# Optimization experiments

Hardware: AMD Instinct MI355X
Metric: run time of the kernel (lower is better)

## Reference

```python
import jax, jax.numpy as jnp
import numpy as np

DIM = 1024
N_HEAD = 16
HEAD_DIM = DIM // N_HEAD
HIDDEN = 4 * DIM
EPS = 1e-6
NEG = -1e9


def setup_inputs() -> dict:
    key = jax.random.key(0)
    ks = jax.random.split(key, 9)
    B, T = 2, 2048
    x = jax.random.normal(ks[0], (B, T, DIM), dtype=jnp.float32)
    # additive causal mask [T, T]
    mask = jnp.where(jnp.tril(jnp.ones((T, T), dtype=bool)), 0.0, NEG).astype(jnp.float32)
    s = 0.02
    wq = jax.random.normal(ks[1], (DIM, DIM), dtype=jnp.float32) * s
    wk = jax.random.normal(ks[2], (DIM, DIM), dtype=jnp.float32) * s
    wv = jax.random.normal(ks[3], (DIM, DIM), dtype=jnp.float32) * s
    wo = jax.random.normal(ks[4], (DIM, DIM), dtype=jnp.float32) * s
    w1 = jax.random.normal(ks[5], (DIM, HIDDEN), dtype=jnp.float32) * s
    w2 = jax.random.normal(ks[6], (HIDDEN, DIM), dtype=jnp.float32) * s
    g_attn = jnp.ones((DIM,), dtype=jnp.float32)
    g_ffn = jnp.ones((DIM,), dtype=jnp.float32)
    return {"x": x, "mask": mask, "wq": wq, "wk": wk, "wv": wv, "wo": wo,
            "w1": w1, "w2": w2, "g_attn": g_attn, "g_ffn": g_ffn}


def _rmsnorm(x, g):
    norm = jax.lax.rsqrt(jnp.mean(jnp.square(x), axis=-1, keepdims=True) + EPS)
    return (x * norm) * g


def _attention(x, mask, wq, wk, wv, wo):
    B, T, C = x.shape
    # project and split heads: [B, H, T, D]
    q = (x @ wq).reshape(B, T, N_HEAD, HEAD_DIM).transpose(0, 2, 1, 3)
    k = (x @ wk).reshape(B, T, N_HEAD, HEAD_DIM).transpose(0, 2, 1, 3)
    v = (x @ wv).reshape(B, T, N_HEAD, HEAD_DIM).transpose(0, 2, 1, 3)
    attn = jnp.einsum('bhtd,bhsd->bhts', q, k) / np.sqrt(HEAD_DIM).astype(np.float32)
    attn = attn + mask  # broadcast [T,T] over [B,H,T,T]
    p = jax.nn.softmax(attn, axis=-1)
    out = jnp.einsum('bhts,bhsd->bhtd', p, v)
    out = out.transpose(0, 2, 1, 3).reshape(B, T, C)
    return out @ wo


def reference(x, mask, wq, wk, wv, wo, w1, w2, g_attn, g_ffn):
    x = x + _attention(_rmsnorm(x, g_attn), mask, wq, wk, wv, wo)
    h = _rmsnorm(x, g_ffn)
    return x + (jax.nn.silu(h @ w1) @ w2)
```

## Files before the change

kernel.cpp:

```cpp
#include <hip/hip_runtime.h>
#include <hip/hip_bf16.h>
#include <cstdint>
#include <cstddef>

#define DIM    1024
#define NHEAD  16
#define HDIM   64
#define HIDDEN 4096
#define TSEQ   2048
#define TOKENS 4096

typedef __attribute__((ext_vector_type(4))) float  f32x4;
typedef __attribute__((ext_vector_type(8))) short  short8;
typedef __attribute__((ext_vector_type(8))) __bf16 bf16x8;

__device__ __forceinline__ short f2bf(float f) {
    union { float f; uint32_t u; } v; v.f = f;
    uint32_t u = v.u;
    uint32_t r = (u + 0x7fffu + ((u >> 16) & 1u)) >> 16;
    return (short)r;
}

__device__ __forceinline__ float bf2f(short s) {
    uint32_t u = ((uint32_t)(uint16_t)s) << 16;
    return __builtin_bit_cast(float, u);
}

__device__ __forceinline__ f32x4 mfma_bf16(short8 a, short8 b, f32x4 c) {
    return __builtin_amdgcn_mfma_f32_16x16x32_bf16(
        __builtin_bit_cast(bf16x8, a), __builtin_bit_cast(bf16x8, b), c, 0, 0, 0);
}

__device__ __forceinline__ void barrier_lds() {
    asm volatile("s_waitcnt lgkmcnt(0)\n\ts_barrier" ::: "memory");
}

__global__ __launch_bounds__(256) void transpose_w(
    const float* __restrict__ W, short* __restrict__ Wt, int K, int N)
{
    __shared__ float tile[64][65];
    const int tid = threadIdx.x;
    const int n0 = blockIdx.x * 64, k0 = blockIdx.y * 64;
    for (int i = tid; i < 4096; i += 256) {
        int r = i >> 6, c = i & 63;
        tile[r][c] = W[(size_t)(k0 + r) * N + n0 + c];
    }
    __syncthreads();
    for (int i = tid; i < 4096; i += 256) {
        int r = i >> 6, c = i & 63;
        Wt[(size_t)(n0 + r) * K + k0 + c] = f2bf(tile[c][r]);
    }
}

__global__ __launch_bounds__(256) void transpose_v(
    const short* __restrict__ qkv, short* __restrict__ Vt)
{
    __shared__ short tile[64][72];
    const int tid = threadIdx.x;
    const int s0 = blockIdx.x * 64, bh = blockIdx.y;
    const int b = bh >> 4, h = bh & 15;
    const short* src = qkv + ((size_t)(b * TSEQ + s0)) * 3072 + 2048 + h * 64;
    for (int i = tid; i < 512; i += 256) {
        int r = i >> 3, cg = i & 7;
        *(short8*)&tile[r][cg * 8] = *(const short8*)(src + (size_t)r * 3072 + cg * 8);
    }
    __syncthreads();
    short* dst = Vt + ((size_t)bh * 64) * TSEQ + s0;
    for (int i = tid; i < 512; i += 256) {
        int d = i >> 3, sg = i & 7;
        short8 o;
#pragma unroll
        for (int j = 0; j < 8; ++j) o[j] = tile[sg * 8 + j][d];
        *(short8*)(dst + (size_t)d * TSEQ + sg * 8) = o;
    }
}

__global__ __launch_bounds__(256) void rmsnorm_k(
    const float* __restrict__ x, const float* __restrict__ g, short* __restrict__ out)
{
    const int t = blockIdx.x, tid = threadIdx.x;
    const int wave = tid >> 6, lane = tid & 63;
    const float4 v = ((const float4*)(x + (size_t)t * DIM))[tid];
    float ss = v.x * v.x + v.y * v.y + v.z * v.z + v.w * v.w;
#pragma unroll
    for (int d = 1; d < 64; d <<= 1) ss += __shfl_xor(ss, d, 64);
    __shared__ float red[4];
    if (lane == 0) red[wave] = ss;
    __syncthreads();
    float tot = red[0] + red[1] + red[2] + red[3];
    float rn = rsqrtf(tot * (1.0f / (float)DIM) + 1e-6f);
    const float4 gv = ((const float4*)g)[tid];
    short4 ov = make_short4(f2bf(v.x * rn * gv.x), f2bf(v.y * rn * gv.y),
                            f2bf(v.z * rn * gv.z), f2bf(v.w * rn * gv.w));
    ((short4*)(out + (size_t)t * DIM))[tid] = ov;
}

template <int EPI>
__global__ __launch_bounds__(256) void gemm_bt(
    const short* __restrict__ A, const short* __restrict__ Bt,
    void* __restrict__ Cout, const float* __restrict__ res,
    int M, int N, int K)
{
    __shared__ short As[128 * 32];
    __shared__ short Bs[128 * 32];
    const int tid  = threadIdx.x;
    const int wave = tid >> 6, lane = tid & 63;
    const int lm = lane & 15, quad = lane >> 4;
    const int wm = wave & 1, wn = wave >> 1;
    const int m0 = blockIdx.x * 128, n0 = blockIdx.y * 128;
    const int Ksl = K / gridDim.z;
    const int kbeg = blockIdx.z * Ksl;
    const int nIter = Ksl >> 5;

    const f32x4 zero = {0.f, 0.f, 0.f, 0.f};
    f32x4 acc[4][4];
#pragma unroll
    for (int i = 0; i < 4; ++i)
#pragma unroll
        for (int j = 0; j < 4; ++j) acc[i][j] = zero;

    const int lrow = wave * 32 + (lane >> 2);
    const int lcol = (lane & 3) * 8;
    const short* Ap = A + (size_t)(m0 + lrow) * K + kbeg + lcol;
    const short* Bp = Bt + (size_t)(n0 + lrow) * K + kbeg + lcol;
    const int woff = lrow * 32 + lcol;

    short8 a00, a01, b00, b01;
    short8 a10, a11, b10, b11;

    auto compute = [&]() {
        short8 af[4], bf[4];
#pragma unroll
        for (int mt = 0; mt < 4; ++mt)
            af[mt] = *(const short8*)&As[(wm * 64 + mt * 16 + lm) * 32 + quad * 8];
#pragma unroll
        for (int nt = 0; nt < 4; ++nt)
            bf[nt] = *(const short8*)&Bs[(wn * 64 + nt * 16 + lm) * 32 + quad * 8];
#pragma unroll
        for (int mt = 0; mt < 4; ++mt)
#pragma unroll
            for (int nt = 0; nt < 4; ++nt)
                acc[mt][nt] = mfma_bf16(af[mt], bf[nt], acc[mt][nt]);
    };

    a00 = *(const short8*)Ap;  a01 = *(const short8*)(Ap + (size_t)16 * K);
    b00 = *(const short8*)Bp;  b01 = *(const short8*)(Bp + (size_t)16 * K);
    Ap += 32; Bp += 32;
    a10 = *(const short8*)Ap;  a11 = *(const short8*)(Ap + (size_t)16 * K);
    b10 = *(const short8*)Bp;  b11 = *(const short8*)(Bp + (size_t)16 * K);
    Ap += 32; Bp += 32;

    for (int it = 0; it < nIter; it += 2) {
        barrier_lds();
        *(short8*)&As[woff] = a00;
        *(short8*)&As[woff + 512] = a01;
        *(short8*)&Bs[woff] = b00;
        *(short8*)&Bs[woff + 512] = b01;
        barrier_lds();
        if (it + 2 < nIter) {
            a00 = *(const short8*)Ap;  a01 = *(const short8*)(Ap + (size_t)16 * K);
            b00 = *(const short8*)Bp;  b01 = *(const short8*)(Bp + (size_t)16 * K);
            Ap += 32; Bp += 32;
        }
        compute();
        barrier_lds();
        *(short8*)&As[woff] = a10;
        *(short8*)&As[woff + 512] = a11;
        *(short8*)&Bs[woff] = b10;
        *(short8*)&Bs[woff + 512] = b11;
        barrier_lds();
        if (it + 3 < nIter) {
            a10 = *(const short8*)Ap;  a11 = *(const short8*)(Ap + (size_t)16 * K);
            b10 = *(const short8*)Bp;  b11 = *(const short8*)(Bp + (size_t)16 * K);
            Ap += 32; Bp += 32;
        }
        compute();
    }

#pragma unroll
    for (int mt = 0; mt < 4; ++mt) {
#pragma unroll
        for (int r = 0; r < 4; ++r) {
            const int row = m0 + wm * 64 + mt * 16 + quad * 4 + r;
#pragma unroll
            for (int nt = 0; nt < 4; ++nt) {
                const int col = n0 + wn * 64 + nt * 16 + lm;
                const size_t idx = (size_t)row * N + col;
                const float v = acc[mt][nt][r];
                if constexpr (EPI == 0) {
                    ((short*)Cout)[idx] = f2bf(v);
                } else if constexpr (EPI == 1) {
                    ((float*)Cout)[idx] = res[idx] + v;
                } else if constexpr (EPI == 2) {
                    ((short*)Cout)[idx] = f2bf(v / (1.0f + __expf(-v)));
                } else {
                    ((short*)Cout)[(size_t)blockIdx.z * M * N + idx] = f2bf(v);
                }
            }
        }
    }
}

__global__ __launch_bounds__(256) void combine_k4(
    const short* __restrict__ p, const float* __restrict__ res,
    float* __restrict__ out, int n)
{
    const int i = blockIdx.x * 256 + threadIdx.x;
    if (i * 4 < n) {
        float4 v = ((const float4*)res)[i];
#pragma unroll
        for (int s = 0; s < 4; ++s) {
            short4 ps = ((const short4*)(p + (size_t)s * n))[i];
            v.x += bf2f(ps.x); v.y += bf2f(ps.y);
            v.z += bf2f(ps.z); v.w += bf2f(ps.w);
        }
        ((float4*)out)[i] = v;
    }
}

__global__ __launch_bounds__(256) void combine_rms4(
    const short* __restrict__ p, const float* __restrict__ res,
    const float* __restrict__ g, float* __restrict__ x2out,
    short* __restrict__ nout)
{
    const int t = blockIdx.x, tid = threadIdx.x;
    const int wave = tid >> 6, lane = tid & 63;
    const size_t i4 = (size_t)t * 256 + tid;
    float4 v = ((const float4*)res)[i4];
#pragma unroll
    for (int s = 0; s < 4; ++s) {
        short4 ps = ((const short4*)(p + (size_t)s * TOKENS * DIM))[i4];
        v.x += bf2f(ps.x); v.y += bf2f(ps.y);
        v.z += bf2f(ps.z); v.w += bf2f(ps.w);
    }
    ((float4*)x2out)[i4] = v;
    float ss = v.x * v.x + v.y * v.y + v.z * v.z + v.w * v.w;
#pragma unroll
    for (int d = 1; d < 64; d <<= 1) ss += __shfl_xor(ss, d, 64);
    __shared__ float red[4];
    if (lane == 0) red[wave] = ss;
    __syncthreads();
    float tot = red[0] + red[1] + red[2] + red[3];
    float rn = rsqrtf(tot * (1.0f / (float)DIM) + 1e-6f);
    const float4 gv = ((const float4*)g)[tid];
    short4 ov = make_short4(f2bf(v.x * rn * gv.x), f2bf(v.y * rn * gv.y),
                            f2bf(v.z * rn * gv.z), f2bf(v.w * rn * gv.w));
    ((short4*)nout)[i4] = ov;
}

#define LP 72
__global__ __launch_bounds__(256, 2) void attn_k(
    const short* __restrict__ qkv, const short* __restrict__ Vt,
    short* __restrict__ out)
{
    __shared__ short Ks[2][64 * LP];
    __shared__ short Vts[2][64 * LP];
    __shared__ short Ps[4][32 * LP];

    const int tid = threadIdx.x, wave = tid >> 6, lane = tid & 63;
    const int pair = wave >> 1, wv = wave & 1;
    const int lm = lane & 15, quad = lane >> 4;
    const int bh = blockIdx.x;
    const int qt = (gridDim.y - 1) - blockIdx.y;
    const int b = bh >> 4, h = bh & 15;
    const int q0 = qt * 64;

    const int n  = qt + 1;
    const int nA = (n + 1) >> 1;
    const int nP = pair ? (n >> 1) : nA;
    const int sbase = pair ? nA : 0;

    const int tp = tid & 127;
    const int rr = tp >> 3, cg = tp & 7;

    const short* qb = qkv + ((size_t)(b * TSEQ + q0)) * 3072 + h * 64;
    short8 aq[2][2];
#pragma unroll
    for (int mt = 0; mt < 2; ++mt)
#pragma unroll
        for (int kk = 0; kk < 2; ++kk)
            aq[mt][kk] = *(const short8*)(qb + (size_t)(wv * 32 + mt * 16 + lm) * 3072 + kk * 32 + quad * 8);

    const short* kb  = qkv + (size_t)b * TSEQ * 3072 + 1024 + h * 64;
    const short* vtb = Vt + (size_t)bh * 64 * TSEQ;

    const f32x4 zero = {0.f, 0.f, 0.f, 0.f};
    f32x4 o_acc[2][4];
#pragma unroll
    for (int mt = 0; mt < 2; ++mt)
#pragma unroll
        for (int t = 0; t < 4; ++t) o_acc[mt][t] = zero;
    float lsum[2][4] = {{0.f, 0.f, 0.f, 0.f}, {0.f, 0.f, 0.f, 0.f}};

    short8 kr[4], vr[4];
    if (nP > 0) {
        const size_t s0 = (size_t)sbase * 64;
#pragma unroll
        for (int j = 0; j < 4; ++j) {
            kr[j] = *(const short8*)(kb + (s0 + rr + j * 16) * 3072 + cg * 8);
            vr[j] = *(const short8*)(vtb + (size_t)(rr + j * 16) * TSEQ + s0 + cg * 8);
        }
    }

    for (int it = 0; it < nA; ++it) {
        const int st = sbase + it;
        const bool act = it < nP;
        __syncthreads();
        if (act) {
#pragma unroll
            for (int j = 0; j < 4; ++j) {
                *(short8*)&Ks[pair][(rr + j * 16) * LP + cg * 8] = kr[j];
                *(short8*)&Vts[pair][(rr + j * 16) * LP + cg * 8] = vr[j];
            }
        }
        __syncthreads();
        if (act && it + 1 < nP) {
            const size_t sn = (size_t)(st + 1) * 64;
#pragma unroll
            for (int j = 0; j < 4; ++j) {
                kr[j] = *(const short8*)(kb + (sn + rr + j * 16) * 3072 + cg * 8);
                vr[j] = *(const short8*)(vtb + (size_t)(rr + j * 16) * TSEQ + sn + cg * 8);
            }
        }
        if (!act) continue;

        f32x4 sa[2][4];
#pragma unroll
        for (int mt = 0; mt < 2; ++mt)
#pragma unroll
            for (int nt = 0; nt < 4; ++nt) sa[mt][nt] = zero;
#pragma unroll
        for (int kk = 0; kk < 2; ++kk) {
#pragma unroll
            for (int nt = 0; nt < 4; ++nt) {
                short8 bk = *(const short8*)&Ks[pair][(nt * 16 + lm) * LP + kk * 32 + quad * 8];
                sa[0][nt] = mfma_bf16(aq[0][kk], bk, sa[0][nt]);
                sa[1][nt] = mfma_bf16(aq[1][kk], bk, sa[1][nt]);
            }
        }

        const int s0 = st * 64;
        const bool band = (st == qt);
#pragma unroll
        for (int mt = 0; mt < 2; ++mt) {
            const int qrow = q0 + wv * 32 + mt * 16 + quad * 4;
#pragma unroll
            for (int nt = 0; nt < 4; ++nt) {
                const int col = s0 + nt * 16 + lm;
#pragma unroll
                for (int r = 0; r < 4; ++r) {
                    float p = __expf(0.125f * sa[mt][nt][r]);
                    if (band && col > qrow + r) p = 0.f;
                    lsum[mt][r] += p;
                    Ps[wave][(mt * 16 + quad * 4 + r) * LP + nt * 16 + lm] =
                        (short)(__builtin_bit_cast(uint32_t, p) >> 16);
                }
            }
        }

#pragma unroll
        for (int kk = 0; kk < 2; ++kk) {
            short8 ap0 = *(const short8*)&Ps[wave][lm * LP + kk * 32 + quad * 8];
            short8 ap1 = *(const short8*)&Ps[wave][(16 + lm) * LP + kk * 32 + quad * 8];
#pragma unroll
            for (int t = 0; t < 4; ++t) {
                short8 bv = *(const short8*)&Vts[pair][(t * 16 + lm) * LP + kk * 32 + quad * 8];
                o_acc[0][t] = mfma_bf16(ap0, bv, o_acc[0][t]);
                o_acc[1][t] = mfma_bf16(ap1, bv, o_acc[1][t]);
            }
        }
    }

#pragma unroll
    for (int mt = 0; mt < 2; ++mt)
#pragma unroll
        for (int r = 0; r < 4; ++r) {
            float s = lsum[mt][r];
#pragma unroll
            for (int d = 1; d < 16; d <<= 1) s += __shfl_xor(s, d, 16);
            lsum[mt][r] = s;
        }

    __syncthreads();
    float* Ob = (float*)&Ks[0][0];
    float* Lb = (float*)&Vts[0][0];
    if (pair == 1) {
#pragma unroll
        for (int mt = 0; mt < 2; ++mt)
#pragma unroll
            for (int t = 0; t < 4; ++t)
#pragma unroll
                for (int r = 0; r < 4; ++r)
                    Ob[(wv * 32 + mt * 16 + quad * 4 + r) * 68 + t * 16 + lm] = o_acc[mt][t][r];
        if (lm == 0) {
#pragma unroll
            for (int mt = 0; mt < 2; ++mt)
#pragma unroll
                for (int r = 0; r < 4; ++r)
                    Lb[wv * 32 + mt * 16 + quad * 4 + r] = lsum[mt][r];
        }
    }
    __syncthreads();
    if (pair == 0) {
#pragma unroll
        for (int mt = 0; mt < 2; ++mt) {
#pragma unroll
            for (int r = 0; r < 4; ++r) {
                const int lrow = wv * 32 + mt * 16 + quad * 4 + r;
                float ltot = lsum[mt][r] + Lb[lrow];
                const float inv = 1.0f / ltot;
                const int token = b * TSEQ + q0 + lrow;
#pragma unroll
                for (int t = 0; t < 4; ++t) {
                    float o = o_acc[mt][t][r] + Ob[lrow * 68 + t * 16 + lm];
                    out[(size_t)token * 1024 + h * 64 + t * 16 + lm] = f2bf(o * inv);
                }
            }
        }
    }
}

extern "C" void kernel_launch(void* const* d_in, const int* in_sizes, int n_in,
                              void* d_out, int out_size, void* d_ws, size_t ws_size,
                              hipStream_t stream)
{
    const float* x      = (const float*)d_in[0];
    const float* wq     = (const float*)d_in[2];
    const float* wk     = (const float*)d_in[3];
    const float* wv     = (const float*)d_in[4];
    const float* wo     = (const float*)d_in[5];
    const float* w1     = (const float*)d_in[6];
    const float* w2     = (const float*)d_in[7];
    const float* g_attn = (const float*)d_in[8];
    const float* g_ffn  = (const float*)d_in[9];
    float* out = (float*)d_out;

    char* ws = (char*)d_ws;
    const size_t MB = 1024 * 1024;
    short* Wqkv_t = (short*)(ws + 0);
    short* Wo_t   = (short*)(ws + 6 * MB);
    short* W1_t   = (short*)(ws + 8 * MB);
    short* xn     = (short*)(ws + 16 * MB);
    short* hbuf   = (short*)(ws + 24 * MB);
    short* qkv    = (short*)(ws + 32 * MB);
    short* pbufO  = (short*)(ws + 32 * MB);
    short* Vt     = (short*)(ws + 64 * MB);
    float* x2     = (float*)(ws + 64 * MB);
    short* W2_t   = (short*)(ws + 80 * MB);
    short* pbuf2  = (short*)(ws + 0);

    dim3 blk(256);

    transpose_w<<<dim3(16, 16), blk, 0, stream>>>(wq, Wqkv_t, 1024, 1024);
    transpose_w<<<dim3(16, 16), blk, 0, stream>>>(wk, Wqkv_t + (size_t)1024 * 1024, 1024, 1024);
    transpose_w<<<dim3(16, 16), blk, 0, stream>>>(wv, Wqkv_t + (size_t)2048 * 1024, 1024, 1024);
    transpose_w<<<dim3(16, 16), blk, 0, stream>>>(wo, Wo_t, 1024, 1024);
    transpose_w<<<dim3(64, 16), blk, 0, stream>>>(w1, W1_t, 1024, 4096);
    transpose_w<<<dim3(16, 64), blk, 0, stream>>>(w2, W2_t, 4096, 1024);

    rmsnorm_k<<<TOKENS, blk, 0, stream>>>(x, g_attn, xn);

    gemm_bt<0><<<dim3(TOKENS / 128, 3072 / 128), blk, 0, stream>>>(
        xn, Wqkv_t, qkv, nullptr, TOKENS, 3072, 1024);

    transpose_v<<<dim3(TSEQ / 64, 32), blk, 0, stream>>>(qkv, Vt);

    attn_k<<<dim3(32, TSEQ / 64), dim3(256), 0, stream>>>(qkv, Vt, xn);

    gemm_bt<3><<<dim3(TOKENS / 128, 1024 / 128, 4), blk, 0, stream>>>(
        xn, Wo_t, pbufO, nullptr, TOKENS, 1024, 1024);

    combine_rms4<<<TOKENS, blk, 0, stream>>>(pbufO, x, g_ffn, x2, hbuf);

    gemm_bt<2><<<dim3(TOKENS / 128, HIDDEN / 128), blk, 0, stream>>>(
        hbuf, W1_t, qkv, nullptr, TOKENS, HIDDEN, 1024);

    gemm_bt<3><<<dim3(TOKENS / 128, 1024 / 128, 4), blk, 0, stream>>>(
        qkv, W2_t, pbuf2, nullptr, TOKENS, 1024, HIDDEN);

    combine_k4<<<dim3(TOKENS * DIM / 4 / 256), blk, 0, stream>>>(
        pbuf2, x2, out, TOKENS * DIM);
}
```

Before: 370.3 us.

## Stage GEMM tiles with direct global-to-LDS loads and double-buffered LDS

Replaces the register-staged global loads and explicit LDS stores in the bf16 GEMM with global_load_lds, which writes straight into LDS. Two LDS buffers let the next K-slice load while the current one is computed, with vmcnt waits to order the two. This removes the VGPR staging and ds_write traffic and may lower register pressure. In exchange it doubles LDS use and depends on the per-wave contiguous layout that the global-to-LDS instruction produces matching the expected tile layout.

```diff
diff --git a/kernel.cpp b/kernel.cpp
--- a/kernel.cpp
+++ b/kernel.cpp
@@ -33,6 +33,13 @@
 
 __device__ __forceinline__ void barrier_lds() {
     asm volatile("s_waitcnt lgkmcnt(0)\n\ts_barrier" ::: "memory");
+}
+
+__device__ __forceinline__ void glds16(const short* g, short* l) {
+    __builtin_amdgcn_global_load_lds(
+        (const __attribute__((address_space(1))) void*)g,
+        (__attribute__((address_space(3))) void*)l,
+        16, 0, 0);
 }
 
 __global__ __launch_bounds__(256) void transpose_w(
@@ -101,8 +108,8 @@
     void* __restrict__ Cout, const float* __restrict__ res,
     int M, int N, int K)
 {
-    __shared__ short As[128 * 32];
-    __shared__ short Bs[128 * 32];
+    __shared__ short As[2][128 * 32];
+    __shared__ short Bs[2][128 * 32];
     const int tid  = threadIdx.x;
     const int wave = tid >> 6, lane = tid & 63;
     const int lm = lane & 15, quad = lane >> 4;
@@ -123,19 +130,25 @@
     const int lcol = (lane & 3) * 8;
     const short* Ap = A + (size_t)(m0 + lrow) * K + kbeg + lcol;
     const short* Bp = Bt + (size_t)(n0 + lrow) * K + kbeg + lcol;
-    const int woff = lrow * 32 + lcol;
-
-    short8 a00, a01, b00, b01;
-    short8 a10, a11, b10, b11;
-
-    auto compute = [&]() {
+
+    auto stage = [&](int buf) {
+        short* a = &As[buf][wave * 1024];
+        short* b = &Bs[buf][wave * 1024];
+        glds16(Ap, a);
+        glds16(Ap + (size_t)16 * K, a + 512);
+        glds16(Bp, b);
+        glds16(Bp + (size_t)16 * K, b + 512);
+        Ap += 32; Bp += 32;
+    };
+
+    auto compute = [&](int buf) {
         short8 af[4], bf[4];
 #pragma unroll
         for (int mt = 0; mt < 4; ++mt)
-            af[mt] = *(const short8*)&As[(wm * 64 + mt * 16 + lm) * 32 + quad * 8];
+            af[mt] = *(const short8*)&As[buf][(wm * 64 + mt * 16 + lm) * 32 + quad * 8];
 #pragma unroll
         for (int nt = 0; nt < 4; ++nt)
-            bf[nt] = *(const short8*)&Bs[(wn * 64 + nt * 16 + lm) * 32 + quad * 8];
+            bf[nt] = *(const short8*)&Bs[buf][(wn * 64 + nt * 16 + lm) * 32 + quad * 8];
 #pragma unroll
         for (int mt = 0; mt < 4; ++mt)
 #pragma unroll
@@ -143,38 +156,18 @@
                 acc[mt][nt] = mfma_bf16(af[mt], bf[nt], acc[mt][nt]);
     };
 
-    a00 = *(const short8*)Ap;  a01 = *(const short8*)(Ap + (size_t)16 * K);
-    b00 = *(const short8*)Bp;  b01 = *(const short8*)(Bp + (size_t)16 * K);
-    Ap += 32; Bp += 32;
-    a10 = *(const short8*)Ap;  a11 = *(const short8*)(Ap + (size_t)16 * K);
-    b10 = *(const short8*)Bp;  b11 = *(const short8*)(Bp + (size_t)16 * K);
-    Ap += 32; Bp += 32;
-
-    for (int it = 0; it < nIter; it += 2) {
+    stage(0);
+
+    for (int it = 0; it < nIter; ++it) {
         barrier_lds();
-        *(short8*)&As[woff] = a00;
-        *(short8*)&As[woff + 512] = a01;
-        *(short8*)&Bs[woff] = b00;
-        *(short8*)&Bs[woff + 512] = b01;
+        if (it + 1 < nIter) {
+            stage((it + 1) & 1);
+            asm volatile("s_waitcnt vmcnt(4)" ::: "memory");
+        } else {
+            asm volatile("s_waitcnt vmcnt(0)" ::: "memory");
+        }
         barrier_lds();
-        if (it + 2 < nIter) {
-            a00 = *(const short8*)Ap;  a01 = *(const short8*)(Ap + (size_t)16 * K);
-            b00 = *(const short8*)Bp;  b01 = *(const short8*)(Bp + (size_t)16 * K);
-            Ap += 32; Bp += 32;
-        }
-        compute();
-        barrier_lds();
-        *(short8*)&As[woff] = a10;
-        *(short8*)&As[woff + 512] = a11;
-        *(short8*)&Bs[woff] = b10;
-        *(short8*)&Bs[woff + 512] = b11;
-        barrier_lds();
-        if (it + 3 < nIter) {
-            a10 = *(const short8*)Ap;  a11 = *(const short8*)(Ap + (size_t)16 * K);
-            b10 = *(const short8*)Bp;  b11 = *(const short8*)(Bp + (size_t)16 * K);
-            Ap += 32; Bp += 32;
-        }
-        compute();
+        compute(it & 1);
     }
 
 #pragma unroll
```

Result: slower. 380.6 us (+2.8%).
